# Kernel tuning notes

Measured on AMD Instinct MI355X. Metric: run time of the kernel, lower is better.

Reference implementation:

```python
import jax, jax.numpy as jnp
import numpy as np

WINDOW_LEN = 512
N_VAR = 64
LOW_RANK = 16
BATCH = 512


def setup_inputs() -> dict:
    key = jax.random.key(0)
    k_x, k_g, k_b, k_A, k_B = jax.random.split(key, 5)
    x = jax.random.normal(k_x, (BATCH, WINDOW_LEN, N_VAR, 1), dtype=jnp.float32)
    # gating initialized at gating_init in the module; use small positive values
    gating = 0.01 * jnp.ones((N_VAR,), dtype=jnp.float32)
    # bias initialized to zeros in the module, but give it random values so the
    # residual path is exercised numerically
    bias = 0.02 * jax.random.normal(k_b, (WINDOW_LEN, N_VAR), dtype=jnp.float32)
    # kaiming-uniform-ish scale for lora_A: bound = sqrt(6 / fan_in) / sqrt(1+a^2) with a=sqrt(5)
    bound = np.sqrt(6.0 / LOW_RANK) / np.sqrt(6.0)
    lora_A = jax.random.uniform(k_A, (WINDOW_LEN, LOW_RANK), dtype=jnp.float32,
                                minval=-bound, maxval=bound)
    # lora_B is zero-init in the module; use small random values for a nontrivial test
    lora_B = 0.02 * jax.random.normal(k_B, (LOW_RANK, WINDOW_LEN, N_VAR), dtype=jnp.float32)
    return {"x": x, "gating": gating, "bias": bias, "lora_A": lora_A, "lora_B": lora_B}


def reference(x, gating, bias, lora_A, lora_B):
    # x: [b, t, n, d] with t == window_len and n*d == n_var (var_wise=True path)
    b, t, n, d = x.shape
    xr = x.reshape(b, t, n * d)                     # [b, t, v]
    x1 = jnp.tanh(gating * xr)                      # gate per variable, [b, t, v]
    # Original computes weight = einsum('ik,kjl->ijl', lora_A, lora_B)  (dense [t,t,v])
    # then einsum('biv,iov->bov', x1, weight). Same math via associativity:
    tmp = jnp.einsum('biv,ik->bkv', x1, lora_A)     # [b, r, v]
    new_x = jnp.einsum('bkv,kov->bov', tmp, lora_B) # [b, t, v]
    out = xr + new_x + bias                          # residual + bias
    return out.reshape(b, t, n, d)
```

## Files before the change

### kernel.cpp

```cpp
#include <hip/hip_runtime.h>

#define WL 512
#define NV 64
#define LR 16
#define NB 512

__device__ __forceinline__ float tanh_fast(float x) {
    float e = __expf(2.0f * x);
    return 1.0f - 2.0f / (e + 1.0f);
}

__global__ __launch_bounds__(512, 4) void k_tmp(
    const float* __restrict__ x, const float* __restrict__ gating,
    const float* __restrict__ A, float* __restrict__ tmp)
{
    __shared__ float red[8 * LR * NV];
    const int tid = threadIdx.x;
    const int b = blockIdx.x;

    const int v = tid & 63;
    const int tg = __builtin_amdgcn_readfirstlane(tid >> 6);
    const float g = gating[v];

    float acc[LR];
#pragma unroll
    for (int k = 0; k < LR; ++k) acc[k] = 0.f;

    const float* xb = x + (size_t)b * (WL * NV) + (size_t)tg * 64 * NV + v;
    const float* Abase = A + (size_t)tg * 64 * LR;

#pragma unroll 4
    for (int i = 0; i < 64; ++i) {
        const float x1 = tanh_fast(g * xb[i * NV]);
        const float* Ar = Abase + i * LR;
#pragma unroll
        for (int k = 0; k < LR; ++k) acc[k] = fmaf(x1, Ar[k], acc[k]);
    }

#pragma unroll
    for (int k = 0; k < LR; ++k) red[(tg * LR + k) * NV + v] = acc[k];
    __syncthreads();
#pragma unroll
    for (int p = tid; p < LR * NV; p += 512) {
        float s = 0.f;
#pragma unroll
        for (int t = 0; t < 8; ++t) s += red[t * (LR * NV) + p];
        tmp[(size_t)b * (LR * NV) + p] = s;
    }
}

__global__ __launch_bounds__(256, 4) void k_out(
    const float* __restrict__ x, const float* __restrict__ bias,
    const float* __restrict__ Bm, const float* __restrict__ tmp,
    float* __restrict__ out)
{
    const int tid = threadIdx.x;
    const int v = tid & 63;
    const int og = tid >> 6;
    const int o_base = blockIdx.y * 16 + og * 4;
    const int b0 = blockIdx.x * 8;

    float Breg[4][LR];
#pragma unroll
    for (int j = 0; j < 4; ++j) {
        const int o = o_base + j;
#pragma unroll
        for (int k = 0; k < LR; ++k)
            Breg[j][k] = Bm[((size_t)k * WL + o) * NV + v];
    }
    float breg[4];
#pragma unroll
    for (int j = 0; j < 4; ++j) breg[j] = bias[(o_base + j) * NV + v];

    for (int bi = 0; bi < 8; ++bi) {
        const int b = b0 + bi;
        const float* tb = tmp + (size_t)b * (LR * NV) + v;
        float tr[LR];
#pragma unroll
        for (int k = 0; k < LR; ++k) tr[k] = tb[k * NV];
        const float* xb = x + (size_t)b * WL * NV;
        float* ob = out + (size_t)b * WL * NV;
#pragma unroll
        for (int j = 0; j < 4; ++j) {
            const int o = o_base + j;
            float acc = breg[j];
#pragma unroll
            for (int k = 0; k < LR; ++k) acc += tr[k] * Breg[j][k];
            ob[o * NV + v] = xb[o * NV + v] + acc;
        }
    }
}

extern "C" void kernel_launch(void* const* d_in, const int* in_sizes, int n_in,
                              void* d_out, int out_size, void* d_ws, size_t ws_size,
                              hipStream_t stream) {
    const float* x      = (const float*)d_in[0];
    const float* gating = (const float*)d_in[1];
    const float* bias   = (const float*)d_in[2];
    const float* A      = (const float*)d_in[3];
    const float* Bm     = (const float*)d_in[4];
    float* out = (float*)d_out;
    float* tmp = (float*)d_ws;

    k_tmp<<<NB, 512, 0, stream>>>(x, gating, A, tmp);
    k_out<<<dim3(64, 32), 256, 0, stream>>>(x, bias, Bm, tmp, out);
}
```

Before: 48.81 us.

## Transpose tmp layout to v-major, prefetch x rows, double batches per block

The partial-sum buffer in k_tmp is padded to stride 17 and written v-major, so k_out can read each variable's 16 rank coefficients as four float4 loads instead of strided scalar loads. k_out now covers 16 batches per block instead of 8, halving the grid and amortizing the B and bias register loads. It also prefetches the next batch's x values into registers to overlap the loads with the FMAs. The cost is fewer blocks in flight and more register pressure.

```diff
diff --git a/kernel.cpp b/kernel.cpp
--- a/kernel.cpp
+++ b/kernel.cpp
@@ -14,7 +14,7 @@
     const float* __restrict__ x, const float* __restrict__ gating,
     const float* __restrict__ A, float* __restrict__ tmp)
 {
-    __shared__ float red[8 * LR * NV];
+    __shared__ float red[8 * NV * 17];
     const int tid = threadIdx.x;
     const int b = blockIdx.x;
 
@@ -37,14 +37,18 @@
         for (int k = 0; k < LR; ++k) acc[k] = fmaf(x1, Ar[k], acc[k]);
     }
 
+    float* rrow = &red[(tg * NV + v) * 17];
 #pragma unroll
-    for (int k = 0; k < LR; ++k) red[(tg * LR + k) * NV + v] = acc[k];
+    for (int k = 0; k < LR; ++k) rrow[k] = acc[k];
     __syncthreads();
+
 #pragma unroll
     for (int p = tid; p < LR * NV; p += 512) {
+        const int v2 = p >> 4;
+        const int k2 = p & 15;
         float s = 0.f;
 #pragma unroll
-        for (int t = 0; t < 8; ++t) s += red[t * (LR * NV) + p];
+        for (int t = 0; t < 8; ++t) s += red[(t * NV + v2) * 17 + k2];
         tmp[(size_t)b * (LR * NV) + p] = s;
     }
 }
@@ -58,7 +62,7 @@
     const int v = tid & 63;
     const int og = tid >> 6;
     const int o_base = blockIdx.y * 16 + og * 4;
-    const int b0 = blockIdx.x * 8;
+    const int b0 = blockIdx.x * 16;
 
     float Breg[4][LR];
 #pragma unroll
@@ -72,21 +76,44 @@
 #pragma unroll
     for (int j = 0; j < 4; ++j) breg[j] = bias[(o_base + j) * NV + v];
 
-    for (int bi = 0; bi < 8; ++bi) {
+    float xr[4], xrn[4];
+    {
+        const float* xb = x + (size_t)b0 * WL * NV;
+#pragma unroll
+        for (int j = 0; j < 4; ++j) xr[j] = xb[(o_base + j) * NV + v];
+    }
+
+    for (int bi = 0; bi < 16; ++bi) {
         const int b = b0 + bi;
-        const float* tb = tmp + (size_t)b * (LR * NV) + v;
+
+        if (bi < 15) {
+            const float* xbn = x + (size_t)(b + 1) * WL * NV;
+#pragma unroll
+            for (int j = 0; j < 4; ++j) xrn[j] = xbn[(o_base + j) * NV + v];
+        }
+
+        const float4* tb4 = (const float4*)(tmp + (size_t)b * (LR * NV) + v * LR);
         float tr[LR];
-#pragma unroll
-        for (int k = 0; k < LR; ++k) tr[k] = tb[k * NV];
-        const float* xb = x + (size_t)b * WL * NV;
+        {
+            float4 t4;
+            t4 = tb4[0]; tr[0]=t4.x; tr[1]=t4.y; tr[2]=t4.z; tr[3]=t4.w;
+            t4 = tb4[1]; tr[4]=t4.x; tr[5]=t4.y; tr[6]=t4.z; tr[7]=t4.w;
+            t4 = tb4[2]; tr[8]=t4.x; tr[9]=t4.y; tr[10]=t4.z; tr[11]=t4.w;
+            t4 = tb4[3]; tr[12]=t4.x; tr[13]=t4.y; tr[14]=t4.z; tr[15]=t4.w;
+        }
+
         float* ob = out + (size_t)b * WL * NV;
 #pragma unroll
         for (int j = 0; j < 4; ++j) {
-            const int o = o_base + j;
             float acc = breg[j];
 #pragma unroll
             for (int k = 0; k < LR; ++k) acc += tr[k] * Breg[j][k];
-            ob[o * NV + v] = xb[o * NV + v] + acc;
+            ob[(o_base + j) * NV + v] = xr[j] + acc;
+        }
+
+        if (bi < 15) {
+#pragma unroll
+            for (int j = 0; j < 4; ++j) xr[j] = xrn[j];
         }
     }
 }
@@ -103,5 +130,5 @@
     float* tmp = (float*)d_ws;
 
     k_tmp<<<NB, 512, 0, stream>>>(x, gating, A, tmp);
-    k_out<<<dim3(64, 32), 256, 0, stream>>>(x, bias, Bm, tmp, out);
+    k_out<<<dim3(32, 32), 256, 0, stream>>>(x, bias, Bm, tmp, out);
 }
```

Result: slower. 50.45 us (+3.4%).
